# Kernel tuning notes

Measured on AMD Instinct MI355X. Metric: run time of the kernel, lower is better.

## Reference

```python
import jax, jax.numpy as jnp
import numpy as np


def setup_inputs() -> dict:
    key = jax.random.key(0)
    ks = jax.random.split(key, 7)
    N, E, H = 100000, 64, 128
    return {
        "U_i": jax.random.normal(ks[0], (N, E), dtype=jnp.float32),
        "W1": jax.random.normal(ks[1], (1, H), dtype=jnp.float32) * (1.0 / 1.0),
        "b1": jax.random.normal(ks[2], (H,), dtype=jnp.float32) * 0.01,
        "W2": jax.random.normal(ks[3], (H, H), dtype=jnp.float32) * (1.0 / np.sqrt(H)),
        "b2": jax.random.normal(ks[4], (H,), dtype=jnp.float32) * 0.01,
        "W3": jax.random.normal(ks[5], (H, 1), dtype=jnp.float32) * (1.0 / np.sqrt(H)),
        "b3": jax.random.normal(ks[6], (1,), dtype=jnp.float32) * 0.01,
    }


def reference(U_i, W1, b1, W2, b2, W3, b3):
    # Pointwise MLP over every scalar of U_i [N, E], then mean over nodes (axis 0).
    # Layer 1 (in_dim=1): U_i[..., None] @ W1 == outer-broadcast with W1[0].
    h = jax.nn.relu(U_i[..., None] * W1[0] + b1)          # [N, E, H]
    h = jax.nn.relu(jnp.einsum("neh,hk->nek", h, W2) + b2)  # [N, E, H]
    y = jnp.einsum("neh,ho->ne", h, W3[:, :]) + b3[0]      # [N, E]
    return jnp.mean(y, axis=0)                              # [E]
```

## Files before the change

### kernel.cpp

```cpp
#include <hip/hip_runtime.h>

#define HH 128
#define TAB_N 4096
#define TAB_LO (-8.0f)
#define TAB_HI (8.0f)
#define NBLK 1024


__global__ __launch_bounds__(256) void build_table_kernel(
    const float* __restrict__ W1, const float* __restrict__ b1,
    const float* __restrict__ W2, const float* __restrict__ b2,
    const float* __restrict__ W3, const float* __restrict__ b3,
    float* __restrict__ table)
{
    __shared__ float4 w2s[HH * 32];
    const int tid = threadIdx.x;

    const float4* W2v = reinterpret_cast<const float4*>(W2);
#pragma unroll
    for (int j = 0; j < 16; ++j)
        w2s[tid + 256 * j] = W2v[tid + 256 * j];
    __syncthreads();

    const int entry = blockIdx.x * 16 + (tid >> 4);
    const int sub   = tid & 15;
    const float step = (TAB_HI - TAB_LO) / (float)(TAB_N - 1);
    const float u = TAB_LO + step * (float)entry;

    float4 a0 = make_float4(0.f, 0.f, 0.f, 0.f);
    float4 a1 = make_float4(0.f, 0.f, 0.f, 0.f);
#pragma unroll 4
    for (int i = 0; i < HH; ++i) {
        const float h1 = fmaxf(fmaf(u, W1[i], b1[i]), 0.0f);
        const float4 w0 = w2s[i * 32 + sub];
        const float4 w1v = w2s[i * 32 + sub + 16];
        a0.x = fmaf(h1, w0.x, a0.x);
        a0.y = fmaf(h1, w0.y, a0.y);
        a0.z = fmaf(h1, w0.z, a0.z);
        a0.w = fmaf(h1, w0.w, a0.w);
        a1.x = fmaf(h1, w1v.x, a1.x);
        a1.y = fmaf(h1, w1v.y, a1.y);
        a1.z = fmaf(h1, w1v.z, a1.z);
        a1.w = fmaf(h1, w1v.w, a1.w);
    }

    const int k0 = 4 * sub;
    const int k1 = 64 + 4 * sub;
    float part = 0.0f;
    part += fmaxf(a0.x + b2[k0 + 0], 0.f) * W3[k0 + 0];
    part += fmaxf(a0.y + b2[k0 + 1], 0.f) * W3[k0 + 1];
    part += fmaxf(a0.z + b2[k0 + 2], 0.f) * W3[k0 + 2];
    part += fmaxf(a0.w + b2[k0 + 3], 0.f) * W3[k0 + 3];
    part += fmaxf(a1.x + b2[k1 + 0], 0.f) * W3[k1 + 0];
    part += fmaxf(a1.y + b2[k1 + 1], 0.f) * W3[k1 + 1];
    part += fmaxf(a1.z + b2[k1 + 2], 0.f) * W3[k1 + 2];
    part += fmaxf(a1.w + b2[k1 + 3], 0.f) * W3[k1 + 3];

    part += __shfl_xor(part, 1, 16);
    part += __shfl_xor(part, 2, 16);
    part += __shfl_xor(part, 4, 16);
    part += __shfl_xor(part, 8, 16);
    if (sub == 0) table[entry] = part + b3[0];
}

__global__ __launch_bounds__(256) void mlp_mean_kernel(
    const float4* __restrict__ U4, const float* __restrict__ table,
    float* __restrict__ partial, int nf4)
{
    __shared__ float tabs[TAB_N];
    __shared__ float4 red[256];
    const int tid = threadIdx.x;

    {
        const float4* tv = reinterpret_cast<const float4*>(table);
        float4* t4 = reinterpret_cast<float4*>(tabs);
#pragma unroll
        for (int j = 0; j < (TAB_N / 4) / 256; ++j)
            t4[tid + 256 * j] = tv[tid + 256 * j];
    }
    __syncthreads();

    const float step = (TAB_HI - TAB_LO) / (float)(TAB_N - 1);
    const float scale = 1.0f / step;
    const float bias = 0.5f - TAB_LO * scale;
    const float tmax = (float)(TAB_N - 1) + 0.49f;

    float4 acc = make_float4(0.f, 0.f, 0.f, 0.f);
    auto accum = [&](float4 v) {
        float t0 = fminf(fmaxf(fmaf(v.x, scale, bias), 0.f), tmax);
        float t1 = fminf(fmaxf(fmaf(v.y, scale, bias), 0.f), tmax);
        float t2 = fminf(fmaxf(fmaf(v.z, scale, bias), 0.f), tmax);
        float t3 = fminf(fmaxf(fmaf(v.w, scale, bias), 0.f), tmax);
        acc.x += tabs[(int)t0];
        acc.y += tabs[(int)t1];
        acc.z += tabs[(int)t2];
        acc.w += tabs[(int)t3];
    };

    const int stride = NBLK * 256;
    int f = blockIdx.x * 256 + tid;
    for (; f + 3 * stride < nf4; f += 4 * stride) {
        float4 v0 = U4[f];
        float4 v1 = U4[f + stride];
        float4 v2 = U4[f + 2 * stride];
        float4 v3 = U4[f + 3 * stride];
        accum(v0); accum(v1); accum(v2); accum(v3);
    }
    for (; f < nf4; f += stride)
        accum(U4[f]);

    red[tid] = acc;
    __syncthreads();

    if (tid < 64) {
        const int g = tid >> 2;
        const int j = tid & 3;
        float s = 0.0f;
#pragma unroll
        for (int m = 0; m < 16; ++m) {
            const float* rp = reinterpret_cast<const float*>(&red[g + 16 * m]);
            s += rp[j];
        }
        partial[blockIdx.x * 64 + tid] = s;
    }
}

__global__ __launch_bounds__(256) void finalize_kernel(
    const float4* __restrict__ partial4, float* __restrict__ out,
    int nblocks, float inv_n)
{
    __shared__ float4 red[256];
    const int tid = threadIdx.x;
    const int q = blockIdx.x;
    float4 s = make_float4(0.f, 0.f, 0.f, 0.f);
    for (int r = tid; r < nblocks; r += 256) {
        float4 v = partial4[r * 16 + q];
        s.x += v.x; s.y += v.y; s.z += v.z; s.w += v.w;
    }
    red[tid] = s;
    __syncthreads();
#pragma unroll
    for (int off = 128; off > 0; off >>= 1) {
        if (tid < off) {
            float4 a = red[tid], b = red[tid + off];
            a.x += b.x; a.y += b.y; a.z += b.z; a.w += b.w;
            red[tid] = a;
        }
        __syncthreads();
    }
    if (tid == 0) {
        float4 t = red[0];
        out[q * 4 + 0] = t.x * inv_n;
        out[q * 4 + 1] = t.y * inv_n;
        out[q * 4 + 2] = t.z * inv_n;
        out[q * 4 + 3] = t.w * inv_n;
    }
}

extern "C" void kernel_launch(void* const* d_in, const int* in_sizes, int n_in,
                              void* d_out, int out_size, void* d_ws, size_t ws_size,
                              hipStream_t stream) {
    const float* U  = (const float*)d_in[0];
    const float* W1 = (const float*)d_in[1];
    const float* b1 = (const float*)d_in[2];
    const float* W2 = (const float*)d_in[3];
    const float* b2 = (const float*)d_in[4];
    const float* W3 = (const float*)d_in[5];
    const float* b3 = (const float*)d_in[6];
    float* out = (float*)d_out;

    float* table   = (float*)d_ws;
    float* partial = (float*)d_ws + TAB_N;

    const int total = in_sizes[0];
    const int n_rows = total / 64;
    const int nf4 = total / 4;

    build_table_kernel<<<TAB_N / 16, 256, 0, stream>>>(
        W1, b1, W2, b2, W3, b3, table);

    mlp_mean_kernel<<<NBLK, 256, 0, stream>>>(
        (const float4*)U, table, partial, nf4);

    finalize_kernel<<<16, 256, 0, stream>>>(
        (const float4*)partial, out, NBLK, 1.0f / (float)n_rows);
}
```

Measured before the change: 20.12 us.

## Keep W2 slices in registers and split the hidden dim across warps in table build

The table-build kernel no longer stages all of W2 in shared memory. Each thread instead holds a 16-row slice of W2 in registers and computes partial layer-2 sums for all 16 table entries of the block. The partials are then reduced across the 8 row groups through shared memory before the bias, ReLU and W3 dot. This removes the 64KB LDS fill and the per-entry LDS reads of W2, at the cost of higher register pressure and an extra LDS reduction pass.

Result: faster. 18.11 us (-10.0%).

```diff
diff --git a/kernel.cpp b/kernel.cpp
--- a/kernel.cpp
+++ b/kernel.cpp
@@ -13,54 +13,77 @@
     const float* __restrict__ W3, const float* __restrict__ b3,
     float* __restrict__ table)
 {
-    __shared__ float4 w2s[HH * 32];
+    __shared__ float4 lds4[16 * 8 * 32];
     const int tid = threadIdx.x;
-
+    const int c  = tid & 31;
+    const int ig = tid >> 5;
+
+    float4 w2r[16];
     const float4* W2v = reinterpret_cast<const float4*>(W2);
 #pragma unroll
-    for (int j = 0; j < 16; ++j)
-        w2s[tid + 256 * j] = W2v[tid + 256 * j];
-    __syncthreads();
-
-    const int entry = blockIdx.x * 16 + (tid >> 4);
-    const int sub   = tid & 15;
+    for (int r = 0; r < 16; ++r)
+        w2r[r] = W2v[(16 * ig + r) * 32 + c];
+
+    float w1r[16], b1r[16];
+#pragma unroll
+    for (int r = 0; r < 16; ++r) {
+        w1r[r] = W1[16 * ig + r];
+        b1r[r] = b1[16 * ig + r];
+    }
+
     const float step = (TAB_HI - TAB_LO) / (float)(TAB_N - 1);
-    const float u = TAB_LO + step * (float)entry;
-
-    float4 a0 = make_float4(0.f, 0.f, 0.f, 0.f);
-    float4 a1 = make_float4(0.f, 0.f, 0.f, 0.f);
-#pragma unroll 4
-    for (int i = 0; i < HH; ++i) {
-        const float h1 = fmaxf(fmaf(u, W1[i], b1[i]), 0.0f);
-        const float4 w0 = w2s[i * 32 + sub];
-        const float4 w1v = w2s[i * 32 + sub + 16];
-        a0.x = fmaf(h1, w0.x, a0.x);
-        a0.y = fmaf(h1, w0.y, a0.y);
-        a0.z = fmaf(h1, w0.z, a0.z);
-        a0.w = fmaf(h1, w0.w, a0.w);
-        a1.x = fmaf(h1, w1v.x, a1.x);
-        a1.y = fmaf(h1, w1v.y, a1.y);
-        a1.z = fmaf(h1, w1v.z, a1.z);
-        a1.w = fmaf(h1, w1v.w, a1.w);
-    }
-
-    const int k0 = 4 * sub;
-    const int k1 = 64 + 4 * sub;
+    const int e0 = blockIdx.x * 16;
+
+    float4 facc[16];
+#pragma unroll
+    for (int e = 0; e < 16; ++e) {
+        const float u = TAB_LO + step * (float)(e0 + e);
+        float4 a = make_float4(0.f, 0.f, 0.f, 0.f);
+#pragma unroll
+        for (int r = 0; r < 16; ++r) {
+            const float h1 = fmaxf(fmaf(u, w1r[r], b1r[r]), 0.0f);
+            a.x = fmaf(h1, w2r[r].x, a.x);
+            a.y = fmaf(h1, w2r[r].y, a.y);
+            a.z = fmaf(h1, w2r[r].z, a.z);
+            a.w = fmaf(h1, w2r[r].w, a.w);
+        }
+        facc[e] = a;
+    }
+
+#pragma unroll
+    for (int e = 0; e < 16; ++e)
+        lds4[(e * 8 + ig) * 32 + c] = facc[e];
+    __syncthreads();
+
+    const float4* b2v = reinterpret_cast<const float4*>(b2);
+    const float4* W3v = reinterpret_cast<const float4*>(W3);
     float part = 0.0f;
-    part += fmaxf(a0.x + b2[k0 + 0], 0.f) * W3[k0 + 0];
-    part += fmaxf(a0.y + b2[k0 + 1], 0.f) * W3[k0 + 1];
-    part += fmaxf(a0.z + b2[k0 + 2], 0.f) * W3[k0 + 2];
-    part += fmaxf(a0.w + b2[k0 + 3], 0.f) * W3[k0 + 3];
-    part += fmaxf(a1.x + b2[k1 + 0], 0.f) * W3[k1 + 0];
-    part += fmaxf(a1.y + b2[k1 + 1], 0.f) * W3[k1 + 1];
-    part += fmaxf(a1.z + b2[k1 + 2], 0.f) * W3[k1 + 2];
-    part += fmaxf(a1.w + b2[k1 + 3], 0.f) * W3[k1 + 3];
-
+#pragma unroll
+    for (int t = 0; t < 2; ++t) {
+        const int cell = 2 * tid + t;
+        const int e  = cell >> 5;
+        const int c2 = cell & 31;
+        float4 s = make_float4(0.f, 0.f, 0.f, 0.f);
+#pragma unroll
+        for (int m = 0; m < 8; ++m) {
+            const float4 v = lds4[(e * 8 + m) * 32 + c2];
+            s.x += v.x; s.y += v.y; s.z += v.z; s.w += v.w;
+        }
+        const float4 bb = b2v[c2];
+        const float4 ww = W3v[c2];
+        float v = 0.0f;
+        v += fmaxf(s.x + bb.x, 0.f) * ww.x;
+        v += fmaxf(s.y + bb.y, 0.f) * ww.y;
+        v += fmaxf(s.z + bb.z, 0.f) * ww.z;
+        v += fmaxf(s.w + bb.w, 0.f) * ww.w;
+        part += v;
+    }
     part += __shfl_xor(part, 1, 16);
     part += __shfl_xor(part, 2, 16);
     part += __shfl_xor(part, 4, 16);
     part += __shfl_xor(part, 8, 16);
-    if (sub == 0) table[entry] = part + b3[0];
+    if ((tid & 15) == 0)
+        table[e0 + (tid >> 4)] = part + b3[0];
 }
 
 __global__ __launch_bounds__(256) void mlp_mean_kernel(
```
